# Performance work log

Hardware: AMD Instinct MI355X
Metric: run time of the kernel (lower is better)

The kernel has to match this reference:

```python
import jax, jax.numpy as jnp
import numpy as np

N_NODES = 50000
N_EDGES = 600000
N_GRAPHS = 1000
IN_DIM = 128   # atom_feat_dim
HID = 128      # emb_dim
NEG_SLOPE = 0.01


def setup_inputs() -> dict:
    key = jax.random.key(0)
    k = jax.random.split(key, 6)
    drug_x = jax.random.normal(k[0], (N_NODES, IN_DIM), dtype=jnp.float32)
    edge_index = jax.random.randint(k[1], (2, N_EDGES), 0, N_NODES, dtype=jnp.int32)
    batch = jnp.sort(jax.random.randint(k[2], (N_NODES,), 0, N_GRAPHS, dtype=jnp.int32))
    # GCNConv parameters (glorot-ish init for weights, zero bias, as in PyG)
    W1 = jax.random.normal(k[3], (IN_DIM, HID), dtype=jnp.float32) * (1.0 / np.sqrt(IN_DIM))
    b1 = jnp.zeros((HID,), dtype=jnp.float32)
    W2 = jax.random.normal(k[4], (HID, HID), dtype=jnp.float32) * (1.0 / np.sqrt(HID))
    b2 = jnp.zeros((HID,), dtype=jnp.float32)
    return {"drug_x": drug_x, "W1": W1, "b1": b1, "W2": W2, "b2": b2,
            "edge_index": edge_index, "batch": batch}


def _gcn_conv(x, W, b, src, dst, n_nodes):
    """PyG GCNConv: lin -> add self-loops -> deg^-1/2 sym norm -> scatter-add -> +bias."""
    h = x @ W  # [N, H]
    ones = jnp.ones(src.shape[0], dtype=h.dtype)
    # degree on the target side, +1 for the self-loop
    deg = jax.ops.segment_sum(ones, dst, num_segments=n_nodes) + 1.0
    dinv = jax.lax.rsqrt(deg)  # [N]
    coef = dinv[src] * dinv[dst]  # [E]
    agg = jax.ops.segment_sum(h[src] * coef[:, None], dst, num_segments=n_nodes)
    # self-loop contribution: dinv[i]*dinv[i]*h[i]
    agg = agg + h * (dinv * dinv)[:, None]
    return agg + b


def _leaky_relu(x):
    return jnp.where(x > 0, x, NEG_SLOPE * x)


def reference(drug_x, W1, b1, W2, b2, edge_index, batch):
    src, dst = edge_index[0], edge_index[1]
    n = drug_x.shape[0]
    h = _leaky_relu(_gcn_conv(drug_x, W1, b1, src, dst, n))  # dropout = identity (eval)
    h = _leaky_relu(_gcn_conv(h, W2, b2, src, dst, n))
    # global_mean_pool over graph ids
    sums = jax.ops.segment_sum(h, batch, num_segments=N_GRAPHS)
    counts = jax.ops.segment_sum(jnp.ones((n,), h.dtype), batch, num_segments=N_GRAPHS)
    return sums / jnp.maximum(counts, 1.0)[:, None]
```

## Files before the change

### kernel.cpp

```cpp
#include <hip/hip_runtime.h>

#define DIM 128
#define NEG_SLOPE 0.01f
#define ELLW 64
#define CPAD 16

typedef short short8 __attribute__((ext_vector_type(8)));
typedef float f32x4 __attribute__((ext_vector_type(4)));

__device__ __forceinline__ unsigned short f2bf(float f) {
    unsigned u = __float_as_uint(f);
    u = u + 0x7FFFu + ((u >> 16) & 1u);
    return (unsigned short)(u >> 16);
}
__device__ __forceinline__ float bf2f(unsigned short s) {
    return __uint_as_float((unsigned)s << 16);
}

__global__ __launch_bounds__(256) void k_fillprep(const int* __restrict__ src,
                                                  const int* __restrict__ dst,
                                                  int* __restrict__ cursorPad,
                                                  int* __restrict__ eSrc,
                                                  const float* __restrict__ W1,
                                                  const float* __restrict__ W2,
                                                  unsigned short* __restrict__ Wt1,
                                                  unsigned short* __restrict__ Wt2,
                                                  int nE) {
    int i = blockIdx.x * 256 + threadIdx.x;
    if (i < nE) {
        int s = src[i], d = dst[i];
        int pos = atomicAdd(&cursorPad[d * CPAD], 1);
        if (pos < ELLW) eSrc[(size_t)d * ELLW + pos] = s;
    }
    if (i < 32768) {
        const float* W = (i < 16384) ? W1 : W2;
        unsigned short* Wt = (i < 16384) ? Wt1 : Wt2;
        int j = i & 16383;
        int k = j >> 7, n = j & 127;
        Wt[n * 128 + k] = f2bf(W[k * 128 + n]);
    }
}

__global__ __launch_bounds__(256) void k_dinv_goff(const int* __restrict__ cursorPad,
                                                   const int* __restrict__ batch,
                                                   float* __restrict__ dinv,
                                                   int* __restrict__ gOff,
                                                   int nN, int nG) {
    int i = blockIdx.x * 256 + threadIdx.x;
    if (i >= nN) return;
    dinv[i] = rsqrtf((float)cursorPad[i * CPAD] + 1.0f);
    int b1 = batch[i];
    int b0 = (i == 0) ? -1 : batch[i - 1];
    for (int g = b0 + 1; g <= b1; ++g) gOff[g] = i;
    if (i == nN - 1) {
        for (int g = b1 + 1; g <= nG; ++g) gOff[g] = nN;
    }
}

#define LDA 136

__global__ __launch_bounds__(256) void k_gemm(const float* __restrict__ X,
                                              const unsigned short* __restrict__ Wt,
                                              const float* __restrict__ dinv,
                                              unsigned short* __restrict__ Y, int nRows) {
    __shared__ unsigned short sA[64 * LDA];
    const int t = threadIdx.x;
    const int row0 = blockIdx.x * 64;

#pragma unroll
    for (int rep = 0; rep < 8; ++rep) {
        int idx = t + rep * 256;
        int r = idx >> 5, k4 = (idx & 31) * 4;
        int gr = row0 + r;
        float4 v = make_float4(0.f, 0.f, 0.f, 0.f);
        if (gr < nRows) v = *(const float4*)&X[(size_t)gr * 128 + k4];
        ushort4 p;
        p.x = f2bf(v.x); p.y = f2bf(v.y); p.z = f2bf(v.z); p.w = f2bf(v.w);
        *(ushort4*)&sA[r * LDA + k4] = p;
    }
    __syncthreads();

    const int wave = t >> 6, lane = t & 63;
    const int l15 = lane & 15;
    const int koff = (lane >> 4) * 8;
    const int arow = wave * 16 + l15;

    short8 a[4];
#pragma unroll
    for (int ks = 0; ks < 4; ++ks)
        a[ks] = *(const short8*)&sA[arow * LDA + ks * 32 + koff];

    f32x4 acc[8];
#pragma unroll
    for (int c = 0; c < 8; ++c) acc[c] = (f32x4){0.f, 0.f, 0.f, 0.f};
#pragma unroll
    for (int c = 0; c < 8; ++c) {
        const unsigned short* wp = Wt + (size_t)(c * 16 + l15) * 128 + koff;
#pragma unroll
        for (int ks = 0; ks < 4; ++ks) {
            short8 b = *(const short8*)(wp + ks * 32);
            acc[c] = __builtin_amdgcn_mfma_f32_16x16x32_bf16(a[ks], b, acc[c], 0, 0, 0);
        }
    }
    const int orow = row0 + wave * 16 + (lane >> 4) * 4;
#pragma unroll
    for (int r = 0; r < 4; ++r) {
        int gr = orow + r;
        if (gr < nRows) {
            float dv = dinv[gr];
#pragma unroll
            for (int c = 0; c < 8; ++c)
                Y[(size_t)gr * 128 + c * 16 + l15] = f2bf(acc[c][r] * dv);
        }
    }
}

__global__ __launch_bounds__(256) void k_gemm_bf(const unsigned short* __restrict__ Xb,
                                                 const unsigned short* __restrict__ Wt,
                                                 const float* __restrict__ dinv,
                                                 unsigned short* __restrict__ Y, int nRows) {
    __shared__ unsigned short sA[64 * LDA];
    const int t = threadIdx.x;
    const int row0 = blockIdx.x * 64;

#pragma unroll
    for (int rep = 0; rep < 4; ++rep) {
        int idx = t + rep * 256;
        int r = idx >> 4, c8 = (idx & 15) * 8;
        int gr = row0 + r;
        uint4 v = make_uint4(0, 0, 0, 0);
        if (gr < nRows) v = *(const uint4*)&Xb[(size_t)gr * 128 + c8];
        *(uint4*)&sA[r * LDA + c8] = v;
    }
    __syncthreads();

    const int wave = t >> 6, lane = t & 63;
    const int l15 = lane & 15;
    const int koff = (lane >> 4) * 8;
    const int arow = wave * 16 + l15;

    short8 a[4];
#pragma unroll
    for (int ks = 0; ks < 4; ++ks)
        a[ks] = *(const short8*)&sA[arow * LDA + ks * 32 + koff];

    f32x4 acc[8];
#pragma unroll
    for (int c = 0; c < 8; ++c) acc[c] = (f32x4){0.f, 0.f, 0.f, 0.f};
#pragma unroll
    for (int c = 0; c < 8; ++c) {
        const unsigned short* wp = Wt + (size_t)(c * 16 + l15) * 128 + koff;
#pragma unroll
        for (int ks = 0; ks < 4; ++ks) {
            short8 b = *(const short8*)(wp + ks * 32);
            acc[c] = __builtin_amdgcn_mfma_f32_16x16x32_bf16(a[ks], b, acc[c], 0, 0, 0);
        }
    }
    const int orow = row0 + wave * 16 + (lane >> 4) * 4;
#pragma unroll
    for (int r = 0; r < 4; ++r) {
        int gr = orow + r;
        if (gr < nRows) {
            float dv = dinv[gr];
#pragma unroll
            for (int c = 0; c < 8; ++c)
                Y[(size_t)gr * 128 + c * 16 + l15] = f2bf(acc[c][r] * dv);
        }
    }
}

#define ACCUM(v)                                         \
    do {                                                 \
        acc[0] += bf2f((v).x & 0xFFFFu);                 \
        acc[1] += __uint_as_float((v).x & 0xFFFF0000u);  \
        acc[2] += bf2f((v).y & 0xFFFFu);                 \
        acc[3] += __uint_as_float((v).y & 0xFFFF0000u);  \
        acc[4] += bf2f((v).z & 0xFFFFu);                 \
        acc[5] += __uint_as_float((v).z & 0xFFFF0000u);  \
        acc[6] += bf2f((v).w & 0xFFFFu);                 \
        acc[7] += __uint_as_float((v).w & 0xFFFF0000u);  \
    } while (0)

__global__ __launch_bounds__(256) void k_gather_bf(const uint4* __restrict__ h4,
                                                   const int* __restrict__ cursorPad,
                                                   const int* __restrict__ eSrc,
                                                   const float* __restrict__ dinv,
                                                   const float* __restrict__ bias,
                                                   unsigned short* __restrict__ outH,
                                                   int n) {
    const int g = threadIdx.x >> 4;
    const int l = threadIdx.x & 15;
    const int i = blockIdx.x * 16 + g;
    if (i >= n) return;
    const int beg = i * ELLW;
    const int deg = min(cursorPad[i * CPAD], ELLW);
    const int end = beg + deg;
    const float di = dinv[i];

    float acc[8];
    {
        uint4 hv = h4[(size_t)i * 16 + l];
        acc[0] = bf2f(hv.x & 0xFFFFu);
        acc[1] = __uint_as_float(hv.x & 0xFFFF0000u);
        acc[2] = bf2f(hv.y & 0xFFFFu);
        acc[3] = __uint_as_float(hv.y & 0xFFFF0000u);
        acc[4] = bf2f(hv.z & 0xFFFFu);
        acc[5] = __uint_as_float(hv.z & 0xFFFF0000u);
        acc[6] = bf2f(hv.w & 0xFFFFu);
        acc[7] = __uint_as_float(hv.w & 0xFFFF0000u);
    }
    int e = beg;
    for (; e + 8 <= end; e += 8) {
        int4 s0 = *(const int4*)&eSrc[e];
        int4 s1 = *(const int4*)&eSrc[e + 4];
        uint4 v[8];
        v[0] = h4[(size_t)s0.x * 16 + l];
        v[1] = h4[(size_t)s0.y * 16 + l];
        v[2] = h4[(size_t)s0.z * 16 + l];
        v[3] = h4[(size_t)s0.w * 16 + l];
        v[4] = h4[(size_t)s1.x * 16 + l];
        v[5] = h4[(size_t)s1.y * 16 + l];
        v[6] = h4[(size_t)s1.z * 16 + l];
        v[7] = h4[(size_t)s1.w * 16 + l];
#pragma unroll
        for (int j = 0; j < 8; ++j) ACCUM(v[j]);
    }
    if (e + 4 <= end) {
        int4 s0 = *(const int4*)&eSrc[e];
        uint4 v[4];
        v[0] = h4[(size_t)s0.x * 16 + l];
        v[1] = h4[(size_t)s0.y * 16 + l];
        v[2] = h4[(size_t)s0.z * 16 + l];
        v[3] = h4[(size_t)s0.w * 16 + l];
#pragma unroll
        for (int j = 0; j < 4; ++j) ACCUM(v[j]);
        e += 4;
    }
    if (e + 2 <= end) {
        int s0 = eSrc[e], s1 = eSrc[e + 1];
        uint4 v0 = h4[(size_t)s0 * 16 + l];
        uint4 v1 = h4[(size_t)s1 * 16 + l];
        ACCUM(v0);
        ACCUM(v1);
        e += 2;
    }
    if (e < end) {
        int s0 = eSrc[e];
        uint4 v0 = h4[(size_t)s0 * 16 + l];
        ACCUM(v0);
    }

    float4 b0 = *(const float4*)&bias[l * 8];
    float4 b1 = *(const float4*)&bias[l * 8 + 4];
    acc[0] = acc[0] * di + b0.x; acc[0] = acc[0] > 0.f ? acc[0] : NEG_SLOPE * acc[0];
    acc[1] = acc[1] * di + b0.y; acc[1] = acc[1] > 0.f ? acc[1] : NEG_SLOPE * acc[1];
    acc[2] = acc[2] * di + b0.z; acc[2] = acc[2] > 0.f ? acc[2] : NEG_SLOPE * acc[2];
    acc[3] = acc[3] * di + b0.w; acc[3] = acc[3] > 0.f ? acc[3] : NEG_SLOPE * acc[3];
    acc[4] = acc[4] * di + b1.x; acc[4] = acc[4] > 0.f ? acc[4] : NEG_SLOPE * acc[4];
    acc[5] = acc[5] * di + b1.y; acc[5] = acc[5] > 0.f ? acc[5] : NEG_SLOPE * acc[5];
    acc[6] = acc[6] * di + b1.z; acc[6] = acc[6] > 0.f ? acc[6] : NEG_SLOPE * acc[6];
    acc[7] = acc[7] * di + b1.w; acc[7] = acc[7] > 0.f ? acc[7] : NEG_SLOPE * acc[7];

    ushort4 p0, p1;
    p0.x = f2bf(acc[0]); p0.y = f2bf(acc[1]); p0.z = f2bf(acc[2]); p0.w = f2bf(acc[3]);
    p1.x = f2bf(acc[4]); p1.y = f2bf(acc[5]); p1.z = f2bf(acc[6]); p1.w = f2bf(acc[7]);
    *(ushort4*)&outH[(size_t)i * 128 + l * 8] = p0;
    *(ushort4*)&outH[(size_t)i * 128 + l * 8 + 4] = p1;
}
#undef ACCUM

__global__ __launch_bounds__(128) void k_pool(const unsigned short* __restrict__ h,
                                              const int* __restrict__ gOff,
                                              float* __restrict__ out, int nG) {
    int g = blockIdx.x;
    int c = threadIdx.x;
    int beg = gOff[g], end = gOff[g + 1];
    float acc = 0.0f;
    for (int r = beg; r < end; ++r) acc += bf2f(h[(size_t)r * DIM + c]);
    float cntf = (float)(end - beg);
    out[(size_t)g * DIM + c] = acc / fmaxf(cntf, 1.0f);
}

extern "C" void kernel_launch(void* const* d_in, const int* in_sizes, int n_in,
                              void* d_out, int out_size, void* d_ws, size_t ws_size,
                              hipStream_t stream) {
    const float* X  = (const float*)d_in[0];
    const float* W1 = (const float*)d_in[1];
    const float* b1 = (const float*)d_in[2];
    const float* W2 = (const float*)d_in[3];
    const float* b2 = (const float*)d_in[4];
    const int*   ei = (const int*)d_in[5];
    const int*   batch = (const int*)d_in[6];
    float* out = (float*)d_out;

    const int NN = in_sizes[0] / DIM;
    const int NE = in_sizes[5] / 2;
    const int NG = out_size / DIM;

    const int* src = ei;
    const int* dst = ei + NE;

    char* ws = (char*)d_ws;
    size_t o = 0;
    auto alloc = [&](size_t bytes) {
        char* p = ws + o;
        o += (bytes + 1023) & ~(size_t)1023;
        return p;
    };
    int* cursorPad = (int*)alloc((size_t)NN * CPAD * 4);
    float* dinv    = (float*)alloc((size_t)NN * 4);
    int*   gOff    = (int*)alloc((size_t)(NG + 1) * 4);
    unsigned short* Wt1 = (unsigned short*)alloc((size_t)16384 * 2);
    unsigned short* Wt2 = (unsigned short*)alloc((size_t)16384 * 2);
    int*   eSrc    = (int*)alloc((size_t)NN * ELLW * 4);
    unsigned short* bufHa = (unsigned short*)alloc((size_t)NN * DIM * 2);
    unsigned short* bufHb = (unsigned short*)alloc((size_t)NN * DIM * 2);

    hipMemsetAsync(cursorPad, 0, (size_t)NN * CPAD * 4, stream);

    const int B = 256;
    const int nb1 = (NN + 255) / 256;

    k_fillprep<<<(NE + B - 1) / B, B, 0, stream>>>(src, dst, cursorPad, eSrc,
                                                   W1, W2, Wt1, Wt2, NE);
    k_dinv_goff<<<nb1, B, 0, stream>>>(cursorPad, batch, dinv, gOff, NN, NG);

    int gemm_grid = (NN + 63) / 64;
    int gather_grid = (NN + 15) / 16;

    k_gemm<<<gemm_grid, B, 0, stream>>>(X, Wt1, dinv, bufHa, NN);
    k_gather_bf<<<gather_grid, B, 0, stream>>>((const uint4*)bufHa, cursorPad, eSrc,
                                               dinv, b1, bufHb, NN);

    k_gemm_bf<<<gemm_grid, B, 0, stream>>>(bufHb, Wt2, dinv, bufHa, NN);
    k_gather_bf<<<gather_grid, B, 0, stream>>>((const uint4*)bufHa, cursorPad, eSrc,
                                               dinv, b2, bufHb, NN);

    k_pool<<<NG, 128, 0, stream>>>(bufHb, gOff, out, NG);
}
```

Measured before the change: 227.1 us.

## Fuse all GCN stages into one cooperative persistent kernel with grid syncs

Replaces the memset plus seven separate launches (fill/prep, dinv/goff, two GEMMs, two gathers, pool) with a single cooperative persistent kernel that runs each stage as a grid-stride loop separated by grid.sync(). The dinv array is dropped and recomputed with rsqrt from the degree counters, and graph offsets are found by binary search over the sorted batch array in the pool stage. The aim is to remove per-launch overhead and small intermediate kernels. In exchange there are six grid-wide barriers, a grid capped at 1024 blocks with persistent loops, and redundant rsqrt and binary-search work.

```diff
diff --git a/kernel.cpp b/kernel.cpp
--- a/kernel.cpp
+++ b/kernel.cpp
@@ -1,9 +1,13 @@
 #include <hip/hip_runtime.h>
+#include <hip/hip_cooperative_groups.h>
+
+namespace cg = cooperative_groups;
 
 #define DIM 128
 #define NEG_SLOPE 0.01f
 #define ELLW 64
 #define CPAD 16
+#define LDA 136
 
 typedef short short8 __attribute__((ext_vector_type(8)));
 typedef float f32x4 __attribute__((ext_vector_type(4)));
@@ -17,156 +21,13 @@
     return __uint_as_float((unsigned)s << 16);
 }
 
-__global__ __launch_bounds__(256) void k_fillprep(const int* __restrict__ src,
-                                                  const int* __restrict__ dst,
-                                                  int* __restrict__ cursorPad,
-                                                  int* __restrict__ eSrc,
-                                                  const float* __restrict__ W1,
-                                                  const float* __restrict__ W2,
-                                                  unsigned short* __restrict__ Wt1,
-                                                  unsigned short* __restrict__ Wt2,
-                                                  int nE) {
-    int i = blockIdx.x * 256 + threadIdx.x;
-    if (i < nE) {
-        int s = src[i], d = dst[i];
-        int pos = atomicAdd(&cursorPad[d * CPAD], 1);
-        if (pos < ELLW) eSrc[(size_t)d * ELLW + pos] = s;
-    }
-    if (i < 32768) {
-        const float* W = (i < 16384) ? W1 : W2;
-        unsigned short* Wt = (i < 16384) ? Wt1 : Wt2;
-        int j = i & 16383;
-        int k = j >> 7, n = j & 127;
-        Wt[n * 128 + k] = f2bf(W[k * 128 + n]);
-    }
-}
-
-__global__ __launch_bounds__(256) void k_dinv_goff(const int* __restrict__ cursorPad,
-                                                   const int* __restrict__ batch,
-                                                   float* __restrict__ dinv,
-                                                   int* __restrict__ gOff,
-                                                   int nN, int nG) {
-    int i = blockIdx.x * 256 + threadIdx.x;
-    if (i >= nN) return;
-    dinv[i] = rsqrtf((float)cursorPad[i * CPAD] + 1.0f);
-    int b1 = batch[i];
-    int b0 = (i == 0) ? -1 : batch[i - 1];
-    for (int g = b0 + 1; g <= b1; ++g) gOff[g] = i;
-    if (i == nN - 1) {
-        for (int g = b1 + 1; g <= nG; ++g) gOff[g] = nN;
-    }
-}
-
-#define LDA 136
-
-__global__ __launch_bounds__(256) void k_gemm(const float* __restrict__ X,
-                                              const unsigned short* __restrict__ Wt,
-                                              const float* __restrict__ dinv,
-                                              unsigned short* __restrict__ Y, int nRows) {
-    __shared__ unsigned short sA[64 * LDA];
-    const int t = threadIdx.x;
-    const int row0 = blockIdx.x * 64;
-
-#pragma unroll
-    for (int rep = 0; rep < 8; ++rep) {
-        int idx = t + rep * 256;
-        int r = idx >> 5, k4 = (idx & 31) * 4;
-        int gr = row0 + r;
-        float4 v = make_float4(0.f, 0.f, 0.f, 0.f);
-        if (gr < nRows) v = *(const float4*)&X[(size_t)gr * 128 + k4];
-        ushort4 p;
-        p.x = f2bf(v.x); p.y = f2bf(v.y); p.z = f2bf(v.z); p.w = f2bf(v.w);
-        *(ushort4*)&sA[r * LDA + k4] = p;
-    }
-    __syncthreads();
-
-    const int wave = t >> 6, lane = t & 63;
-    const int l15 = lane & 15;
-    const int koff = (lane >> 4) * 8;
-    const int arow = wave * 16 + l15;
-
-    short8 a[4];
-#pragma unroll
-    for (int ks = 0; ks < 4; ++ks)
-        a[ks] = *(const short8*)&sA[arow * LDA + ks * 32 + koff];
-
-    f32x4 acc[8];
-#pragma unroll
-    for (int c = 0; c < 8; ++c) acc[c] = (f32x4){0.f, 0.f, 0.f, 0.f};
-#pragma unroll
-    for (int c = 0; c < 8; ++c) {
-        const unsigned short* wp = Wt + (size_t)(c * 16 + l15) * 128 + koff;
-#pragma unroll
-        for (int ks = 0; ks < 4; ++ks) {
-            short8 b = *(const short8*)(wp + ks * 32);
-            acc[c] = __builtin_amdgcn_mfma_f32_16x16x32_bf16(a[ks], b, acc[c], 0, 0, 0);
-        }
-    }
-    const int orow = row0 + wave * 16 + (lane >> 4) * 4;
-#pragma unroll
-    for (int r = 0; r < 4; ++r) {
-        int gr = orow + r;
-        if (gr < nRows) {
-            float dv = dinv[gr];
-#pragma unroll
-            for (int c = 0; c < 8; ++c)
-                Y[(size_t)gr * 128 + c * 16 + l15] = f2bf(acc[c][r] * dv);
-        }
-    }
-}
-
-__global__ __launch_bounds__(256) void k_gemm_bf(const unsigned short* __restrict__ Xb,
-                                                 const unsigned short* __restrict__ Wt,
-                                                 const float* __restrict__ dinv,
-                                                 unsigned short* __restrict__ Y, int nRows) {
-    __shared__ unsigned short sA[64 * LDA];
-    const int t = threadIdx.x;
-    const int row0 = blockIdx.x * 64;
-
-#pragma unroll
-    for (int rep = 0; rep < 4; ++rep) {
-        int idx = t + rep * 256;
-        int r = idx >> 4, c8 = (idx & 15) * 8;
-        int gr = row0 + r;
-        uint4 v = make_uint4(0, 0, 0, 0);
-        if (gr < nRows) v = *(const uint4*)&Xb[(size_t)gr * 128 + c8];
-        *(uint4*)&sA[r * LDA + c8] = v;
-    }
-    __syncthreads();
-
-    const int wave = t >> 6, lane = t & 63;
-    const int l15 = lane & 15;
-    const int koff = (lane >> 4) * 8;
-    const int arow = wave * 16 + l15;
-
-    short8 a[4];
-#pragma unroll
-    for (int ks = 0; ks < 4; ++ks)
-        a[ks] = *(const short8*)&sA[arow * LDA + ks * 32 + koff];
-
-    f32x4 acc[8];
-#pragma unroll
-    for (int c = 0; c < 8; ++c) acc[c] = (f32x4){0.f, 0.f, 0.f, 0.f};
-#pragma unroll
-    for (int c = 0; c < 8; ++c) {
-        const unsigned short* wp = Wt + (size_t)(c * 16 + l15) * 128 + koff;
-#pragma unroll
-        for (int ks = 0; ks < 4; ++ks) {
-            short8 b = *(const short8*)(wp + ks * 32);
-            acc[c] = __builtin_amdgcn_mfma_f32_16x16x32_bf16(a[ks], b, acc[c], 0, 0, 0);
-        }
-    }
-    const int orow = row0 + wave * 16 + (lane >> 4) * 4;
-#pragma unroll
-    for (int r = 0; r < 4; ++r) {
-        int gr = orow + r;
-        if (gr < nRows) {
-            float dv = dinv[gr];
-#pragma unroll
-            for (int c = 0; c < 8; ++c)
-                Y[(size_t)gr * 128 + c * 16 + l15] = f2bf(acc[c][r] * dv);
-        }
-    }
+__device__ __forceinline__ int lower_bound_i(const int* __restrict__ a, int n, int key) {
+    int lo = 0, hi = n;
+    while (lo < hi) {
+        int mid = (lo + hi) >> 1;
+        if (a[mid] < key) lo = mid + 1; else hi = mid;
+    }
+    return lo;
 }
 
 #define ACCUM(v)                                         \
@@ -181,21 +42,17 @@
         acc[7] += __uint_as_float((v).w & 0xFFFF0000u);  \
     } while (0)
 
-__global__ __launch_bounds__(256) void k_gather_bf(const uint4* __restrict__ h4,
-                                                   const int* __restrict__ cursorPad,
-                                                   const int* __restrict__ eSrc,
-                                                   const float* __restrict__ dinv,
-                                                   const float* __restrict__ bias,
-                                                   unsigned short* __restrict__ outH,
-                                                   int n) {
-    const int g = threadIdx.x >> 4;
-    const int l = threadIdx.x & 15;
-    const int i = blockIdx.x * 16 + g;
-    if (i >= n) return;
+__device__ __forceinline__ void gather_one(const uint4* __restrict__ h4,
+                                           const int* __restrict__ cursorPad,
+                                           const int* __restrict__ eSrc,
+                                           const float* __restrict__ bias,
+                                           unsigned short* __restrict__ outH,
+                                           int i, int l) {
     const int beg = i * ELLW;
-    const int deg = min(cursorPad[i * CPAD], ELLW);
+    const int cnt = cursorPad[i * CPAD];
+    const int deg = min(cnt, ELLW);
     const int end = beg + deg;
-    const float di = dinv[i];
+    const float di = rsqrtf((float)cnt + 1.0f);
 
     float acc[8];
     {
@@ -267,38 +124,189 @@
     *(ushort4*)&outH[(size_t)i * 128 + l * 8] = p0;
     *(ushort4*)&outH[(size_t)i * 128 + l * 8 + 4] = p1;
 }
+
+__global__ __launch_bounds__(256, 4) void k_mega(
+    const int* __restrict__ src, const int* __restrict__ dst,
+    const int* __restrict__ batch,
+    const float* __restrict__ X,
+    const float* __restrict__ W1, const float* __restrict__ b1,
+    const float* __restrict__ W2, const float* __restrict__ b2,
+    float* __restrict__ out,
+    int* __restrict__ cursorPad,
+    unsigned short* __restrict__ Wt1, unsigned short* __restrict__ Wt2,
+    int* __restrict__ eSrc,
+    unsigned short* __restrict__ bufHa, unsigned short* __restrict__ bufHb,
+    int nN, int nE, int nG)
+{
+    cg::grid_group grid = cg::this_grid();
+    __shared__ unsigned short sA[64 * LDA];
+    const int t = threadIdx.x;
+    const int bid = blockIdx.x;
+    const int nB = gridDim.x;
+    const int gstride = nB * 256;
+    const int gtid = bid * 256 + t;
+
+    for (int i = gtid; i < nN * CPAD; i += gstride) cursorPad[i] = 0;
+    grid.sync();
+
+    for (int i = gtid; i < nE; i += gstride) {
+        int s = src[i], d = dst[i];
+        int pos = atomicAdd(&cursorPad[d * CPAD], 1);
+        if (pos < ELLW) eSrc[(size_t)d * ELLW + pos] = s;
+    }
+    for (int i = gtid; i < 32768; i += gstride) {
+        const float* W = (i < 16384) ? W1 : W2;
+        unsigned short* Wt = (i < 16384) ? Wt1 : Wt2;
+        int j = i & 16383;
+        int k = j >> 7, n = j & 127;
+        Wt[n * 128 + k] = f2bf(W[k * 128 + n]);
+    }
+    grid.sync();
+
+    const int wave = t >> 6, lane = t & 63;
+    const int l15 = lane & 15;
+    const int koff = (lane >> 4) * 8;
+    const int arow = wave * 16 + l15;
+    const int nTiles = (nN + 63) >> 6;
+
+    for (int tile = bid; tile < nTiles; tile += nB) {
+        const int row0 = tile << 6;
+        __syncthreads();
+#pragma unroll
+        for (int rep = 0; rep < 8; ++rep) {
+            int idx = t + rep * 256;
+            int r = idx >> 5, k4 = (idx & 31) * 4;
+            int gr = row0 + r;
+            float4 v = make_float4(0.f, 0.f, 0.f, 0.f);
+            if (gr < nN) v = *(const float4*)&X[(size_t)gr * 128 + k4];
+            ushort4 p;
+            p.x = f2bf(v.x); p.y = f2bf(v.y); p.z = f2bf(v.z); p.w = f2bf(v.w);
+            *(ushort4*)&sA[r * LDA + k4] = p;
+        }
+        __syncthreads();
+
+        short8 a[4];
+#pragma unroll
+        for (int ks = 0; ks < 4; ++ks)
+            a[ks] = *(const short8*)&sA[arow * LDA + ks * 32 + koff];
+
+        f32x4 acc[8];
+#pragma unroll
+        for (int c = 0; c < 8; ++c) acc[c] = (f32x4){0.f, 0.f, 0.f, 0.f};
+#pragma unroll
+        for (int c = 0; c < 8; ++c) {
+            const unsigned short* wp = Wt1 + (size_t)(c * 16 + l15) * 128 + koff;
+#pragma unroll
+            for (int ks = 0; ks < 4; ++ks) {
+                short8 b = *(const short8*)(wp + ks * 32);
+                acc[c] = __builtin_amdgcn_mfma_f32_16x16x32_bf16(a[ks], b, acc[c], 0, 0, 0);
+            }
+        }
+        const int orow = row0 + wave * 16 + (lane >> 4) * 4;
+#pragma unroll
+        for (int r = 0; r < 4; ++r) {
+            int gr = orow + r;
+            if (gr < nN) {
+                float dv = rsqrtf((float)cursorPad[gr * CPAD] + 1.0f);
+#pragma unroll
+                for (int c = 0; c < 8; ++c)
+                    bufHa[(size_t)gr * 128 + c * 16 + l15] = f2bf(acc[c][r] * dv);
+            }
+        }
+    }
+    grid.sync();
+
+    for (int base = bid * 16; base < nN; base += nB * 16) {
+        int i = base + (t >> 4);
+        if (i < nN)
+            gather_one((const uint4*)bufHa, cursorPad, eSrc, b1, bufHb, i, t & 15);
+    }
+    grid.sync();
+
+    for (int tile = bid; tile < nTiles; tile += nB) {
+        const int row0 = tile << 6;
+        __syncthreads();
+#pragma unroll
+        for (int rep = 0; rep < 4; ++rep) {
+            int idx = t + rep * 256;
+            int r = idx >> 4, c8 = (idx & 15) * 8;
+            int gr = row0 + r;
+            uint4 v = make_uint4(0, 0, 0, 0);
+            if (gr < nN) v = *(const uint4*)&bufHb[(size_t)gr * 128 + c8];
+            *(uint4*)&sA[r * LDA + c8] = v;
+        }
+        __syncthreads();
+
+        short8 a[4];
+#pragma unroll
+        for (int ks = 0; ks < 4; ++ks)
+            a[ks] = *(const short8*)&sA[arow * LDA + ks * 32 + koff];
+
+        f32x4 acc[8];
+#pragma unroll
+        for (int c = 0; c < 8; ++c) acc[c] = (f32x4){0.f, 0.f, 0.f, 0.f};
+#pragma unroll
+        for (int c = 0; c < 8; ++c) {
+            const unsigned short* wp = Wt2 + (size_t)(c * 16 + l15) * 128 + koff;
+#pragma unroll
+            for (int ks = 0; ks < 4; ++ks) {
+                short8 b = *(const short8*)(wp + ks * 32);
+                acc[c] = __builtin_amdgcn_mfma_f32_16x16x32_bf16(a[ks], b, acc[c], 0, 0, 0);
+            }
+        }
+        const int orow = row0 + wave * 16 + (lane >> 4) * 4;
+#pragma unroll
+        for (int r = 0; r < 4; ++r) {
+            int gr = orow + r;
+            if (gr < nN) {
+                float dv = rsqrtf((float)cursorPad[gr * CPAD] + 1.0f);
+#pragma unroll
+                for (int c = 0; c < 8; ++c)
+                    bufHa[(size_t)gr * 128 + c * 16 + l15] = f2bf(acc[c][r] * dv);
+            }
+        }
+    }
+    grid.sync();
+
+    for (int base = bid * 16; base < nN; base += nB * 16) {
+        int i = base + (t >> 4);
+        if (i < nN)
+            gather_one((const uint4*)bufHa, cursorPad, eSrc, b2, bufHb, i, t & 15);
+    }
+    grid.sync();
+
+    for (int base = bid * 2; base < nG; base += nB * 2) {
+        int g = base + (t >> 7);
+        if (g < nG) {
+            int beg = lower_bound_i(batch, nN, g);
+            int end = lower_bound_i(batch, nN, g + 1);
+            int c = t & 127;
+            float acc = 0.0f;
+            for (int r = beg; r < end; ++r) acc += bf2f(bufHb[(size_t)r * DIM + c]);
+            out[(size_t)g * DIM + c] = acc / fmaxf((float)(end - beg), 1.0f);
+        }
+    }
+}
 #undef ACCUM
-
-__global__ __launch_bounds__(128) void k_pool(const unsigned short* __restrict__ h,
-                                              const int* __restrict__ gOff,
-                                              float* __restrict__ out, int nG) {
-    int g = blockIdx.x;
-    int c = threadIdx.x;
-    int beg = gOff[g], end = gOff[g + 1];
-    float acc = 0.0f;
-    for (int r = beg; r < end; ++r) acc += bf2f(h[(size_t)r * DIM + c]);
-    float cntf = (float)(end - beg);
-    out[(size_t)g * DIM + c] = acc / fmaxf(cntf, 1.0f);
-}
 
 extern "C" void kernel_launch(void* const* d_in, const int* in_sizes, int n_in,
                               void* d_out, int out_size, void* d_ws, size_t ws_size,
                               hipStream_t stream) {
+    const int* ei = (const int*)d_in[5];
+
+    int NN = in_sizes[0] / DIM;
+    int NE = in_sizes[5] / 2;
+    int NG = out_size / DIM;
+
+    const int* src = ei;
+    const int* dst = ei + NE;
+    const int* batch = (const int*)d_in[6];
     const float* X  = (const float*)d_in[0];
     const float* W1 = (const float*)d_in[1];
     const float* b1 = (const float*)d_in[2];
     const float* W2 = (const float*)d_in[3];
     const float* b2 = (const float*)d_in[4];
-    const int*   ei = (const int*)d_in[5];
-    const int*   batch = (const int*)d_in[6];
     float* out = (float*)d_out;
-
-    const int NN = in_sizes[0] / DIM;
-    const int NE = in_sizes[5] / 2;
-    const int NG = out_size / DIM;
-
-    const int* src = ei;
-    const int* dst = ei + NE;
 
     char* ws = (char*)d_ws;
     size_t o = 0;
@@ -308,33 +316,25 @@
         return p;
     };
     int* cursorPad = (int*)alloc((size_t)NN * CPAD * 4);
-    float* dinv    = (float*)alloc((size_t)NN * 4);
-    int*   gOff    = (int*)alloc((size_t)(NG + 1) * 4);
     unsigned short* Wt1 = (unsigned short*)alloc((size_t)16384 * 2);
     unsigned short* Wt2 = (unsigned short*)alloc((size_t)16384 * 2);
-    int*   eSrc    = (int*)alloc((size_t)NN * ELLW * 4);
+    int* eSrc = (int*)alloc((size_t)NN * ELLW * 4);
     unsigned short* bufHa = (unsigned short*)alloc((size_t)NN * DIM * 2);
     unsigned short* bufHb = (unsigned short*)alloc((size_t)NN * DIM * 2);
 
-    hipMemsetAsync(cursorPad, 0, (size_t)NN * CPAD * 4, stream);
-
-    const int B = 256;
-    const int nb1 = (NN + 255) / 256;
-
-    k_fillprep<<<(NE + B - 1) / B, B, 0, stream>>>(src, dst, cursorPad, eSrc,
-                                                   W1, W2, Wt1, Wt2, NE);
-    k_dinv_goff<<<nb1, B, 0, stream>>>(cursorPad, batch, dinv, gOff, NN, NG);
-
-    int gemm_grid = (NN + 63) / 64;
-    int gather_grid = (NN + 15) / 16;
-
-    k_gemm<<<gemm_grid, B, 0, stream>>>(X, Wt1, dinv, bufHa, NN);
-    k_gather_bf<<<gather_grid, B, 0, stream>>>((const uint4*)bufHa, cursorPad, eSrc,
-                                               dinv, b1, bufHb, NN);
-
-    k_gemm_bf<<<gemm_grid, B, 0, stream>>>(bufHb, Wt2, dinv, bufHa, NN);
-    k_gather_bf<<<gather_grid, B, 0, stream>>>((const uint4*)bufHa, cursorPad, eSrc,
-                                               dinv, b2, bufHb, NN);
-
-    k_pool<<<NG, 128, 0, stream>>>(bufHb, gOff, out, NG);
-}
+    int maxBlocksPerCU = 0;
+    hipOccupancyMaxActiveBlocksPerMultiprocessor(&maxBlocksPerCU, k_mega, 256, 0);
+    if (maxBlocksPerCU < 1) maxBlocksPerCU = 1;
+    int grid = maxBlocksPerCU * 256;
+    if (grid > 1024) grid = 1024;
+
+    void* args[] = {
+        (void*)&src, (void*)&dst, (void*)&batch, (void*)&X,
+        (void*)&W1, (void*)&b1, (void*)&W2, (void*)&b2,
+        (void*)&out, (void*)&cursorPad, (void*)&Wt1, (void*)&Wt2,
+        (void*)&eSrc, (void*)&bufHa, (void*)&bufHb,
+        (void*)&NN, (void*)&NE, (void*)&NG
+    };
+    hipLaunchCooperativeKernel((const void*)k_mega, dim3(grid), dim3(256),
+                               args, 0, stream);
+}
```

Measured after the change: 604.0 us. +166.0%, slower.
